# Optimization experiments

Hardware: AMD Instinct MI355X
Metric: run time of the kernel (lower is better)

## Reference

```python
import jax, jax.numpy as jnp
import numpy as np

N_GRAPHS, NODES_PER, DEG, D = 128, 1024, 32, 256
N = N_GRAPHS * NODES_PER          # 131072 nodes
E = N * DEG                       # 4194304 edges
RATIO = 0.8
K = int(np.ceil(RATIO * NODES_PER))  # 820 nodes kept per graph


def setup_inputs() -> dict:
    key = jax.random.key(0)
    k1, k2, k3, k4 = jax.random.split(key, 4)
    x = jax.random.normal(k1, (N, D), dtype=jnp.float32)
    # intra-graph random edges: endpoints within [0, NODES_PER) + graph offset
    src = jax.random.randint(k2, (E,), 0, NODES_PER)
    dst = jax.random.randint(k3, (E,), 0, NODES_PER)
    goff = (jnp.arange(E) // (NODES_PER * DEG)) * NODES_PER
    edge_index = jnp.stack([src + goff, dst + goff]).astype(jnp.int32)
    batch = jnp.repeat(jnp.arange(N_GRAPHS, dtype=jnp.int32), NODES_PER)
    W = jax.random.normal(k4, (D, 1), dtype=jnp.float32) / np.sqrt(D)
    b = jnp.zeros((1,), dtype=jnp.float32)
    return {"x": x, "edge_index": edge_index, "batch": batch, "W": W, "b": b}


def _gcn_score(x, edge_index, W, b):
    # GCNConv(in_channels, 1) with added self-loops and symmetric normalization
    n = x.shape[0]
    row, col = edge_index[0], edge_index[1]  # source, target
    # degree at target, init 1.0 accounts for self-loop
    deg = jnp.ones((n,), x.dtype).at[col].add(jnp.ones_like(col, dtype=x.dtype))
    dinv = jax.lax.rsqrt(deg)
    h = x @ W                                 # [n, 1]
    norm = dinv[row] * dinv[col]              # [E]
    agg = jnp.zeros_like(h).at[col].add(norm[:, None] * h[row])
    agg = agg + (dinv * dinv)[:, None] * h    # self-loop contribution deg^-1 * h_i
    return (agg + b).squeeze(-1)              # [n]


def reference(x, edge_index, batch, W, b):
    score = _gcn_score(x, edge_index, W, b)                     # [N]
    # per-graph top-k (graphs are contiguous, equal size)
    score_g = score.reshape(N_GRAPHS, NODES_PER)
    _, idx = jax.lax.top_k(score_g, K)                          # [G, K]
    perm = (idx + jnp.arange(N_GRAPHS)[:, None] * NODES_PER).reshape(-1)  # [G*K]
    x_new = x[perm] * jnp.tanh(score[perm])[:, None]            # [G*K, D]
    batch_new = batch[perm]
    # filter_adj: remap kept nodes to new ids, mask edges with dropped endpoints
    new_id = jnp.full((x.shape[0],), -1, dtype=perm.dtype).at[perm].set(
        jnp.arange(perm.shape[0], dtype=perm.dtype))
    r2 = new_id[edge_index[0]]
    c2 = new_id[edge_index[1]]
    edge_mask = (r2 >= 0) & (c2 >= 0)                           # [E] valid edges
    edge_index_new = jnp.where(edge_mask, jnp.stack([r2, c2]), -1)  # [2, E], -1 = dropped
    return x_new, edge_index_new, edge_mask, batch_new, perm
```

## Files before the change

kernel.cpp:

```cpp
#include <hip/hip_runtime.h>
#include <math.h>

constexpr int NG    = 128;
constexpr int NP    = 1024;
constexpr int D     = 256;
constexpr int NTOT  = NG * NP;
constexpr int EPG   = NP * 32;
constexpr int ET    = NTOT * 32;
constexpr int KK    = 820;
constexpr int NKEEP = NG * KK;
constexpr int BPG   = 4;
constexpr int EPB   = EPG / BPG;
constexpr int NBE   = NG * BPG;

constexpr int K1_BLOCKS = 2048;
constexpr int K3_BLOCKS = 2048;

typedef float v4f __attribute__((ext_vector_type(4)));

constexpr long long OUT_X     = 0;
constexpr long long OUT_EI0   = (long long)NKEEP * D;
constexpr long long OUT_EI1   = OUT_EI0 + ET;
constexpr long long OUT_MASK  = OUT_EI0 + 2LL * ET;
constexpr long long OUT_BATCH = OUT_MASK + ET;
constexpr long long OUT_PERM  = OUT_BATCH + NKEEP;

__global__ __launch_bounds__(256) void k1_h(const float* __restrict__ x,
                                            const float* __restrict__ W,
                                            float* __restrict__ h,
                                            int* __restrict__ new_id) {
    const int t    = threadIdx.x;
    const int w    = t >> 6;
    const int lane = t & 63;
    const int gw   = blockIdx.x * 4 + w;

    float4 w4 = ((const float4*)W)[lane];
    const float4* xp = (const float4*)(x + (size_t)gw * 16 * D);

#pragma unroll
    for (int c = 0; c < 4; ++c) {
        float4 a0 = xp[(c * 4 + 0) * 64 + lane];
        float4 a1 = xp[(c * 4 + 1) * 64 + lane];
        float4 a2 = xp[(c * 4 + 2) * 64 + lane];
        float4 a3 = xp[(c * 4 + 3) * 64 + lane];
        float s0 = a0.x * w4.x + a0.y * w4.y + a0.z * w4.z + a0.w * w4.w;
        float s1 = a1.x * w4.x + a1.y * w4.y + a1.z * w4.z + a1.w * w4.w;
        float s2 = a2.x * w4.x + a2.y * w4.y + a2.z * w4.z + a2.w * w4.w;
        float s3 = a3.x * w4.x + a3.y * w4.y + a3.z * w4.z + a3.w * w4.w;
#pragma unroll
        for (int off = 32; off > 0; off >>= 1) {
            s0 += __shfl_down(s0, off, 64);
            s1 += __shfl_down(s1, off, 64);
            s2 += __shfl_down(s2, off, 64);
            s3 += __shfl_down(s3, off, 64);
        }
        if (lane == 0) {
            const int r = gw * 16 + c * 4;
            h[r] = s0; h[r + 1] = s1; h[r + 2] = s2; h[r + 3] = s3;
            new_id[r]     = -1; new_id[r + 1] = -1;
            new_id[r + 2] = -1; new_id[r + 3] = -1;
        }
    }
}

__global__ __launch_bounds__(1024) void k2_graph(
        const float* __restrict__ h,  const float* __restrict__ bptr,
        const int* __restrict__ rows, const int* __restrict__ cols,
        int* __restrict__ perm_i,     int* __restrict__ new_id,
        float* __restrict__ factor,
        float* __restrict__ out_perm, float* __restrict__ out_batch) {
    __shared__ unsigned long long sk[NP];
    __shared__ float acc[NP];
    __shared__ float scl[NP];
    int*   cnt = (int*)sk;
    float* ul  = (float*)sk + NP;

    const int g = blockIdx.x;
    const int t = threadIdx.x;

    const float hv = h[g * NP + t];
    cnt[t] = 0;
    __syncthreads();

    const int4* c4 = (const int4*)(cols + (size_t)g * EPG);
    const int4* r4 = (const int4*)(rows + (size_t)g * EPG);

#pragma unroll
    for (int i = t; i < EPG / 4; i += 1024) {
        int4 c = c4[i];
        atomicAdd(&cnt[c.x & (NP - 1)], 1);
        atomicAdd(&cnt[c.y & (NP - 1)], 1);
        atomicAdd(&cnt[c.z & (NP - 1)], 1);
        atomicAdd(&cnt[c.w & (NP - 1)], 1);
    }
    __syncthreads();

    const float di = rsqrtf((float)(1 + cnt[t]));
    ul[t]  = di * hv;
    acc[t] = 0.0f;
    __syncthreads();

#pragma unroll
    for (int i = t; i < EPG / 4; i += 1024) {
        int4 c = c4[i];
        int4 r = r4[i];
        atomicAdd(&acc[c.x & (NP - 1)], ul[r.x & (NP - 1)]);
        atomicAdd(&acc[c.y & (NP - 1)], ul[r.y & (NP - 1)]);
        atomicAdd(&acc[c.z & (NP - 1)], ul[r.z & (NP - 1)]);
        atomicAdd(&acc[c.w & (NP - 1)], ul[r.w & (NP - 1)]);
    }
    __syncthreads();

    const float score = di * acc[t] + di * di * hv + bptr[0];
    scl[t] = score;

    unsigned int fu = __float_as_uint(score);
    unsigned int s  = (fu & 0x80000000u) ? ~fu : (fu | 0x80000000u);
    unsigned long long key = ((unsigned long long)(~s) << 32) | (unsigned int)t;

    for (int k = 2; k <= NP; k <<= 1) {
        for (int j = k >> 1; j > 0; j >>= 1) {
            unsigned long long other;
            if (j < 64) {
                other = __shfl_xor(key, j, 64);
            } else {
                sk[t] = key;
                __syncthreads();
                other = sk[t ^ j];
                __syncthreads();
            }
            bool take_min = (((t & k) == 0) == ((t & j) == 0));
            bool omin = other < key;
            key = (take_min == omin) ? other : key;
        }
    }

    if (t < KK) {
        int idx  = (int)(key & 0xFFFFFFFFull);
        int node = g * NP + idx;
        int j    = g * KK + t;
        perm_i[j]    = node;
        new_id[node] = j;
        out_perm[j]  = (float)node;
        out_batch[j] = (float)g;
        factor[j]    = tanhf(scl[idx]);
    }
}

__global__ __launch_bounds__(256) void k3_gather_edge(
        const float* __restrict__ x,
        const int* __restrict__ rows, const int* __restrict__ cols,
        const int* __restrict__ new_id,
        const int* __restrict__ perm_i, const float* __restrict__ factor,
        float* __restrict__ out) {
    __shared__ int nid[NP];
    const int b    = blockIdx.x;
    const int t    = threadIdx.x;
    const int w    = t >> 6;
    const int lane = t & 63;

    if (b < NBE) {
        const int g = b >> 2;
        for (int i = t; i < NP; i += 256) nid[i] = new_id[g * NP + i];
        __syncthreads();
        size_t eoff = (size_t)g * EPG + (size_t)(b & 3) * EPB;
        const int4* r4 = (const int4*)(rows + eoff);
        const int4* c4 = (const int4*)(cols + eoff);
        v4f* orr = (v4f*)(out + OUT_EI0  + eoff);
        v4f* occ = (v4f*)(out + OUT_EI1  + eoff);
        v4f* omm = (v4f*)(out + OUT_MASK + eoff);
#pragma unroll
        for (int i = t; i < EPB / 4; i += 256) {
            int4 r = r4[i];
            int4 c = c4[i];
            v4f fr, fc, fm;
            {
                int nr = nid[r.x & (NP - 1)], nc = nid[c.x & (NP - 1)];
                bool m = (nr >= 0) && (nc >= 0);
                fr.x = m ? (float)nr : -1.0f; fc.x = m ? (float)nc : -1.0f; fm.x = m ? 1.0f : 0.0f;
            }
            {
                int nr = nid[r.y & (NP - 1)], nc = nid[c.y & (NP - 1)];
                bool m = (nr >= 0) && (nc >= 0);
                fr.y = m ? (float)nr : -1.0f; fc.y = m ? (float)nc : -1.0f; fm.y = m ? 1.0f : 0.0f;
            }
            {
                int nr = nid[r.z & (NP - 1)], nc = nid[c.z & (NP - 1)];
                bool m = (nr >= 0) && (nc >= 0);
                fr.z = m ? (float)nr : -1.0f; fc.z = m ? (float)nc : -1.0f; fm.z = m ? 1.0f : 0.0f;
            }
            {
                int nr = nid[r.w & (NP - 1)], nc = nid[c.w & (NP - 1)];
                bool m = (nr >= 0) && (nc >= 0);
                fr.w = m ? (float)nr : -1.0f; fc.w = m ? (float)nc : -1.0f; fm.w = m ? 1.0f : 0.0f;
            }
            __builtin_nontemporal_store(fr, &orr[i]);
            __builtin_nontemporal_store(fc, &occ[i]);
            __builtin_nontemporal_store(fm, &omm[i]);
        }
    } else {
        const int gw = (b - NBE) * 4 + w;
        for (int j = gw; j < NKEEP; j += (K3_BLOCKS - NBE) * 4) {
            const int node = perm_i[j];
            const float f  = factor[j];
            float4 v = ((const float4*)(x + (size_t)node * D))[lane];
            v4f o;
            o.x = v.x * f; o.y = v.y * f; o.z = v.z * f; o.w = v.w * f;
            __builtin_nontemporal_store(o, &((v4f*)(out + OUT_X + (size_t)j * D))[lane]);
        }
    }
}

extern "C" void kernel_launch(void* const* d_in, const int* in_sizes, int n_in,
                              void* d_out, int out_size, void* d_ws, size_t ws_size,
                              hipStream_t stream) {
    (void)in_sizes; (void)n_in; (void)out_size; (void)ws_size;

    const float* x  = (const float*)d_in[0];
    const int*   ei = (const int*)d_in[1];
    const float* W  = (const float*)d_in[3];
    const float* b  = (const float*)d_in[4];
    float* out = (float*)d_out;

    float* wsf      = (float*)d_ws;
    float* h        = wsf;
    int*   new_id   = (int*)(wsf + NTOT);
    int*   perm_i   = (int*)(wsf + 2 * NTOT);
    float* factor   = wsf + 2 * NTOT + NKEEP;

    const int* rows = ei;
    const int* cols = ei + ET;

    hipLaunchKernelGGL(k1_h, dim3(K1_BLOCKS), dim3(256), 0, stream,
                       x, W, h, new_id);
    hipLaunchKernelGGL(k2_graph, dim3(NG), dim3(1024), 0, stream,
                       h, b, rows, cols, perm_i, new_id, factor,
                       out + OUT_PERM, out + OUT_BATCH);
    hipLaunchKernelGGL(k3_gather_edge, dim3(K3_BLOCKS), dim3(256), 0, stream,
                       x, rows, cols, new_id, perm_i, factor, out);
}
```

Measured before the change: 350.5 us.

## Fuse score, top-k, gather and edge filter into one per-graph kernel

```diff
diff --git a/kernel.cpp b/kernel.cpp
--- a/kernel.cpp
+++ b/kernel.cpp
@@ -8,13 +8,9 @@
 constexpr int EPG   = NP * 32;
 constexpr int ET    = NTOT * 32;
 constexpr int KK    = 820;
+constexpr int KH    = KK / 2;
 constexpr int NKEEP = NG * KK;
-constexpr int BPG   = 4;
-constexpr int EPB   = EPG / BPG;
-constexpr int NBE   = NG * BPG;
-
-constexpr int K1_BLOCKS = 2048;
-constexpr int K3_BLOCKS = 2048;
+constexpr int EHALF = EPG / 2;
 
 typedef float v4f __attribute__((ext_vector_type(4)));
 
@@ -25,69 +21,66 @@
 constexpr long long OUT_BATCH = OUT_MASK + ET;
 constexpr long long OUT_PERM  = OUT_BATCH + NKEEP;
 
-__global__ __launch_bounds__(256) void k1_h(const float* __restrict__ x,
-                                            const float* __restrict__ W,
-                                            float* __restrict__ h,
-                                            int* __restrict__ new_id) {
+__global__ __launch_bounds__(1024) void sagpool_fused(
+        const float* __restrict__ x,   const float* __restrict__ W,
+        const float* __restrict__ bptr,
+        const int* __restrict__ rows,  const int* __restrict__ cols,
+        float* __restrict__ out) {
+    __shared__ float h_lds[NP];
+    __shared__ unsigned long long sk[NP];
+    __shared__ float acc[NP];
+    __shared__ float scl[NP];
+    __shared__ int   nid[NP];
+    int*   cnt  = (int*)sk;
+    float* ul   = (float*)sk + NP;
+    int*   kidx = (int*)h_lds;
+    float* kfac = acc;
+
+    const int blk  = blockIdx.x;
     const int t    = threadIdx.x;
     const int w    = t >> 6;
     const int lane = t & 63;
-    const int gw   = blockIdx.x * 4 + w;
-
-    float4 w4 = ((const float4*)W)[lane];
-    const float4* xp = (const float4*)(x + (size_t)gw * 16 * D);
-
-#pragma unroll
-    for (int c = 0; c < 4; ++c) {
-        float4 a0 = xp[(c * 4 + 0) * 64 + lane];
-        float4 a1 = xp[(c * 4 + 1) * 64 + lane];
-        float4 a2 = xp[(c * 4 + 2) * 64 + lane];
-        float4 a3 = xp[(c * 4 + 3) * 64 + lane];
-        float s0 = a0.x * w4.x + a0.y * w4.y + a0.z * w4.z + a0.w * w4.w;
-        float s1 = a1.x * w4.x + a1.y * w4.y + a1.z * w4.z + a1.w * w4.w;
-        float s2 = a2.x * w4.x + a2.y * w4.y + a2.z * w4.z + a2.w * w4.w;
-        float s3 = a3.x * w4.x + a3.y * w4.y + a3.z * w4.z + a3.w * w4.w;
-#pragma unroll
-        for (int off = 32; off > 0; off >>= 1) {
-            s0 += __shfl_down(s0, off, 64);
-            s1 += __shfl_down(s1, off, 64);
-            s2 += __shfl_down(s2, off, 64);
-            s3 += __shfl_down(s3, off, 64);
-        }
-        if (lane == 0) {
-            const int r = gw * 16 + c * 4;
-            h[r] = s0; h[r + 1] = s1; h[r + 2] = s2; h[r + 3] = s3;
-            new_id[r]     = -1; new_id[r + 1] = -1;
-            new_id[r + 2] = -1; new_id[r + 3] = -1;
-        }
-    }
-}
-
-__global__ __launch_bounds__(1024) void k2_graph(
-        const float* __restrict__ h,  const float* __restrict__ bptr,
-        const int* __restrict__ rows, const int* __restrict__ cols,
-        int* __restrict__ perm_i,     int* __restrict__ new_id,
-        float* __restrict__ factor,
-        float* __restrict__ out_perm, float* __restrict__ out_batch) {
-    __shared__ unsigned long long sk[NP];
-    __shared__ float acc[NP];
-    __shared__ float scl[NP];
-    int*   cnt = (int*)sk;
-    float* ul  = (float*)sk + NP;
-
-    const int g = blockIdx.x;
-    const int t = threadIdx.x;
-
-    const float hv = h[g * NP + t];
+    const int g    = blk >> 1;
+    const int half = blk & 1;
+
     cnt[t] = 0;
-    __syncthreads();
-
-    const int4* c4 = (const int4*)(cols + (size_t)g * EPG);
-    const int4* r4 = (const int4*)(rows + (size_t)g * EPG);
+    nid[t] = -1;
+
+    {
+        float4 w4 = ((const float4*)W)[lane];
+        const float4* xp = (const float4*)(x + (size_t)g * NP * D);
+#pragma unroll
+        for (int c = 0; c < 16; ++c) {
+            const int r0 = w * 64 + c * 4;
+            float4 a0 = xp[(r0 + 0) * 64 + lane];
+            float4 a1 = xp[(r0 + 1) * 64 + lane];
+            float4 a2 = xp[(r0 + 2) * 64 + lane];
+            float4 a3 = xp[(r0 + 3) * 64 + lane];
+            float s0 = a0.x * w4.x + a0.y * w4.y + a0.z * w4.z + a0.w * w4.w;
+            float s1 = a1.x * w4.x + a1.y * w4.y + a1.z * w4.z + a1.w * w4.w;
+            float s2 = a2.x * w4.x + a2.y * w4.y + a2.z * w4.z + a2.w * w4.w;
+            float s3 = a3.x * w4.x + a3.y * w4.y + a3.z * w4.z + a3.w * w4.w;
+#pragma unroll
+            for (int off = 32; off > 0; off >>= 1) {
+                s0 += __shfl_down(s0, off, 64);
+                s1 += __shfl_down(s1, off, 64);
+                s2 += __shfl_down(s2, off, 64);
+                s3 += __shfl_down(s3, off, 64);
+            }
+            if (lane == 0) {
+                h_lds[r0]     = s0; h_lds[r0 + 1] = s1;
+                h_lds[r0 + 2] = s2; h_lds[r0 + 3] = s3;
+            }
+        }
+    }
+    __syncthreads();
+
+    const int4* c4p = (const int4*)(cols + (size_t)g * EPG);
+    const int4* r4p = (const int4*)(rows + (size_t)g * EPG);
 
 #pragma unroll
     for (int i = t; i < EPG / 4; i += 1024) {
-        int4 c = c4[i];
+        int4 c = c4p[i];
         atomicAdd(&cnt[c.x & (NP - 1)], 1);
         atomicAdd(&cnt[c.y & (NP - 1)], 1);
         atomicAdd(&cnt[c.z & (NP - 1)], 1);
@@ -95,6 +88,7 @@
     }
     __syncthreads();
 
+    const float hv = h_lds[t];
     const float di = rsqrtf((float)(1 + cnt[t]));
     ul[t]  = di * hv;
     acc[t] = 0.0f;
@@ -102,8 +96,8 @@
 
 #pragma unroll
     for (int i = t; i < EPG / 4; i += 1024) {
-        int4 c = c4[i];
-        int4 r = r4[i];
+        int4 c = c4p[i];
+        int4 r = r4p[i];
         atomicAdd(&acc[c.x & (NP - 1)], ul[r.x & (NP - 1)]);
         atomicAdd(&acc[c.y & (NP - 1)], ul[r.y & (NP - 1)]);
         atomicAdd(&acc[c.z & (NP - 1)], ul[r.z & (NP - 1)]);
@@ -137,40 +131,37 @@
 
     if (t < KK) {
         int idx  = (int)(key & 0xFFFFFFFFull);
-        int node = g * NP + idx;
-        int j    = g * KK + t;
-        perm_i[j]    = node;
-        new_id[node] = j;
-        out_perm[j]  = (float)node;
-        out_batch[j] = (float)g;
-        factor[j]    = tanhf(scl[idx]);
-    }
-}
-
-__global__ __launch_bounds__(256) void k3_gather_edge(
-        const float* __restrict__ x,
-        const int* __restrict__ rows, const int* __restrict__ cols,
-        const int* __restrict__ new_id,
-        const int* __restrict__ perm_i, const float* __restrict__ factor,
-        float* __restrict__ out) {
-    __shared__ int nid[NP];
-    const int b    = blockIdx.x;
-    const int t    = threadIdx.x;
-    const int w    = t >> 6;
-    const int lane = t & 63;
-
-    if (b < NBE) {
-        const int g = b >> 2;
-        for (int i = t; i < NP; i += 256) nid[i] = new_id[g * NP + i];
-        __syncthreads();
-        size_t eoff = (size_t)g * EPG + (size_t)(b & 3) * EPB;
+        nid[idx] = g * KK + t;
+        if (t >= half * KH && t < half * KH + KH) {
+            const int l = t - half * KH;
+            kidx[l] = idx;
+            kfac[l] = tanhf(scl[idx]);
+            const int jj = g * KK + t;
+            out[OUT_PERM + jj]  = (float)(g * NP + idx);
+            out[OUT_BATCH + jj] = (float)g;
+        }
+    }
+    __syncthreads();
+
+    for (int l = w; l < KH; l += 16) {
+        const int   ni = kidx[l];
+        const float f  = kfac[l];
+        float4 v = ((const float4*)(x + ((size_t)(g * NP + ni)) * D))[lane];
+        v4f o;
+        o.x = v.x * f; o.y = v.y * f; o.z = v.z * f; o.w = v.w * f;
+        const size_t j = (size_t)g * KK + half * KH + l;
+        __builtin_nontemporal_store(o, &((v4f*)(out + OUT_X + j * D))[lane]);
+    }
+
+    {
+        const size_t eoff = (size_t)g * EPG + (size_t)half * EHALF;
         const int4* r4 = (const int4*)(rows + eoff);
         const int4* c4 = (const int4*)(cols + eoff);
         v4f* orr = (v4f*)(out + OUT_EI0  + eoff);
         v4f* occ = (v4f*)(out + OUT_EI1  + eoff);
         v4f* omm = (v4f*)(out + OUT_MASK + eoff);
 #pragma unroll
-        for (int i = t; i < EPB / 4; i += 256) {
+        for (int i = t; i < EHALF / 4; i += 1024) {
             int4 r = r4[i];
             int4 c = c4[i];
             v4f fr, fc, fm;
@@ -198,23 +189,13 @@
             __builtin_nontemporal_store(fc, &occ[i]);
             __builtin_nontemporal_store(fm, &omm[i]);
         }
-    } else {
-        const int gw = (b - NBE) * 4 + w;
-        for (int j = gw; j < NKEEP; j += (K3_BLOCKS - NBE) * 4) {
-            const int node = perm_i[j];
-            const float f  = factor[j];
-            float4 v = ((const float4*)(x + (size_t)node * D))[lane];
-            v4f o;
-            o.x = v.x * f; o.y = v.y * f; o.z = v.z * f; o.w = v.w * f;
-            __builtin_nontemporal_store(o, &((v4f*)(out + OUT_X + (size_t)j * D))[lane]);
-        }
     }
 }
 
 extern "C" void kernel_launch(void* const* d_in, const int* in_sizes, int n_in,
                               void* d_out, int out_size, void* d_ws, size_t ws_size,
                               hipStream_t stream) {
-    (void)in_sizes; (void)n_in; (void)out_size; (void)ws_size;
+    (void)in_sizes; (void)n_in; (void)out_size; (void)d_ws; (void)ws_size;
 
     const float* x  = (const float*)d_in[0];
     const int*   ei = (const int*)d_in[1];
@@ -222,20 +203,9 @@
     const float* b  = (const float*)d_in[4];
     float* out = (float*)d_out;
 
-    float* wsf      = (float*)d_ws;
-    float* h        = wsf;
-    int*   new_id   = (int*)(wsf + NTOT);
-    int*   perm_i   = (int*)(wsf + 2 * NTOT);
-    float* factor   = wsf + 2 * NTOT + NKEEP;
-
     const int* rows = ei;
     const int* cols = ei + ET;
 
-    hipLaunchKernelGGL(k1_h, dim3(K1_BLOCKS), dim3(256), 0, stream,
-                       x, W, h, new_id);
-    hipLaunchKernelGGL(k2_graph, dim3(NG), dim3(1024), 0, stream,
-                       h, b, rows, cols, perm_i, new_id, factor,
-                       out + OUT_PERM, out + OUT_BATCH);
-    hipLaunchKernelGGL(k3_gather_edge, dim3(K3_BLOCKS), dim3(256), 0, stream,
-                       x, rows, cols, new_id, perm_i, factor, out);
+    hipLaunchKernelGGL(sagpool_fused, dim3(2 * NG), dim3(1024), 0, stream,
+                       x, W, b, rows, cols, out);
 }
```

After: 348.5 us. About the same (-0.6%).

## Move degree counting into the first kernel alongside the x@W projection

Applied to the files above, without the earlier changes.

```diff
diff --git a/kernel.cpp b/kernel.cpp
--- a/kernel.cpp
+++ b/kernel.cpp
@@ -13,7 +13,9 @@
 constexpr int EPB   = EPG / BPG;
 constexpr int NBE   = NG * BPG;
 
-constexpr int K1_BLOCKS = 2048;
+constexpr int K1_DEG    = NG;
+constexpr int K1_HBLK   = 2048;
+constexpr int K1_BLOCKS = K1_DEG + K1_HBLK;
 constexpr int K3_BLOCKS = 2048;
 
 typedef float v4f __attribute__((ext_vector_type(4)));
@@ -25,18 +27,40 @@
 constexpr long long OUT_BATCH = OUT_MASK + ET;
 constexpr long long OUT_PERM  = OUT_BATCH + NKEEP;
 
-__global__ __launch_bounds__(256) void k1_h(const float* __restrict__ x,
-                                            const float* __restrict__ W,
-                                            float* __restrict__ h,
-                                            int* __restrict__ new_id) {
-    const int t    = threadIdx.x;
+__global__ __launch_bounds__(256) void k1_h_deg(const float* __restrict__ x,
+                                                const float* __restrict__ W,
+                                                const int* __restrict__ cols,
+                                                float* __restrict__ h,
+                                                float* __restrict__ dinv) {
+    __shared__ int cnt[NP];
+    const int b = blockIdx.x;
+    const int t = threadIdx.x;
+
+    if (b < K1_DEG) {
+        const int g = b;
+        for (int i = t; i < NP; i += 256) cnt[i] = 0;
+        __syncthreads();
+        const int4* c4 = (const int4*)(cols + (size_t)g * EPG);
+#pragma unroll
+        for (int i = t; i < EPG / 4; i += 256) {
+            int4 c = c4[i];
+            atomicAdd(&cnt[c.x & (NP - 1)], 1);
+            atomicAdd(&cnt[c.y & (NP - 1)], 1);
+            atomicAdd(&cnt[c.z & (NP - 1)], 1);
+            atomicAdd(&cnt[c.w & (NP - 1)], 1);
+        }
+        __syncthreads();
+        for (int i = t; i < NP; i += 256)
+            dinv[g * NP + i] = rsqrtf((float)(1 + cnt[i]));
+        return;
+    }
+
+    const int bb   = b - K1_DEG;
     const int w    = t >> 6;
     const int lane = t & 63;
-    const int gw   = blockIdx.x * 4 + w;
-
+    const int gw   = bb * 4 + w;
     float4 w4 = ((const float4*)W)[lane];
     const float4* xp = (const float4*)(x + (size_t)gw * 16 * D);
-
 #pragma unroll
     for (int c = 0; c < 4; ++c) {
         float4 a0 = xp[(c * 4 + 0) * 64 + lane];
@@ -57,49 +81,33 @@
         if (lane == 0) {
             const int r = gw * 16 + c * 4;
             h[r] = s0; h[r + 1] = s1; h[r + 2] = s2; h[r + 3] = s3;
-            new_id[r]     = -1; new_id[r + 1] = -1;
-            new_id[r + 2] = -1; new_id[r + 3] = -1;
         }
     }
 }
 
 __global__ __launch_bounds__(1024) void k2_graph(
-        const float* __restrict__ h,  const float* __restrict__ bptr,
-        const int* __restrict__ rows, const int* __restrict__ cols,
-        int* __restrict__ perm_i,     int* __restrict__ new_id,
-        float* __restrict__ factor,
-        float* __restrict__ out_perm, float* __restrict__ out_batch) {
+        const float* __restrict__ h,    const float* __restrict__ dinv,
+        const float* __restrict__ bptr,
+        const int* __restrict__ rows,   const int* __restrict__ cols,
+        int* __restrict__ perm_i,       float* __restrict__ factor,
+        int* __restrict__ new_id,
+        float* __restrict__ out_perm,   float* __restrict__ out_batch) {
     __shared__ unsigned long long sk[NP];
     __shared__ float acc[NP];
     __shared__ float scl[NP];
-    int*   cnt = (int*)sk;
-    float* ul  = (float*)sk + NP;
+    float* ul = (float*)sk;
 
     const int g = blockIdx.x;
     const int t = threadIdx.x;
 
     const float hv = h[g * NP + t];
-    cnt[t] = 0;
+    const float dv = dinv[g * NP + t];
+    ul[t]  = dv * hv;
+    acc[t] = 0.0f;
     __syncthreads();
 
     const int4* c4 = (const int4*)(cols + (size_t)g * EPG);
     const int4* r4 = (const int4*)(rows + (size_t)g * EPG);
-
-#pragma unroll
-    for (int i = t; i < EPG / 4; i += 1024) {
-        int4 c = c4[i];
-        atomicAdd(&cnt[c.x & (NP - 1)], 1);
-        atomicAdd(&cnt[c.y & (NP - 1)], 1);
-        atomicAdd(&cnt[c.z & (NP - 1)], 1);
-        atomicAdd(&cnt[c.w & (NP - 1)], 1);
-    }
-    __syncthreads();
-
-    const float di = rsqrtf((float)(1 + cnt[t]));
-    ul[t]  = di * hv;
-    acc[t] = 0.0f;
-    __syncthreads();
-
 #pragma unroll
     for (int i = t; i < EPG / 4; i += 1024) {
         int4 c = c4[i];
@@ -111,7 +119,7 @@
     }
     __syncthreads();
 
-    const float score = di * acc[t] + di * di * hv + bptr[0];
+    const float score = dv * acc[t] + dv * dv * hv + bptr[0];
     scl[t] = score;
 
     unsigned int fu = __float_as_uint(score);
@@ -135,15 +143,16 @@
         }
     }
 
+    const int idx = (int)(key & 0xFFFFFFFFull);
     if (t < KK) {
-        int idx  = (int)(key & 0xFFFFFFFFull);
-        int node = g * NP + idx;
-        int j    = g * KK + t;
-        perm_i[j]    = node;
-        new_id[node] = j;
-        out_perm[j]  = (float)node;
-        out_batch[j] = (float)g;
-        factor[j]    = tanhf(scl[idx]);
+        const int jj = g * KK + t;
+        new_id[g * NP + idx] = jj;
+        perm_i[jj]   = g * NP + idx;
+        factor[jj]   = tanhf(scl[idx]);
+        out_perm[jj]  = (float)(g * NP + idx);
+        out_batch[jj] = (float)g;
+    } else {
+        new_id[g * NP + idx] = -1;
     }
 }
 
@@ -224,17 +233,18 @@
 
     float* wsf      = (float*)d_ws;
     float* h        = wsf;
-    int*   new_id   = (int*)(wsf + NTOT);
-    int*   perm_i   = (int*)(wsf + 2 * NTOT);
-    float* factor   = wsf + 2 * NTOT + NKEEP;
+    float* dinv     = wsf + NTOT;
+    int*   new_id   = (int*)(wsf + 2 * NTOT);
+    int*   perm_i   = (int*)(wsf + 3 * NTOT);
+    float* factor   = wsf + 3 * NTOT + NKEEP;
 
     const int* rows = ei;
     const int* cols = ei + ET;
 
-    hipLaunchKernelGGL(k1_h, dim3(K1_BLOCKS), dim3(256), 0, stream,
-                       x, W, h, new_id);
+    hipLaunchKernelGGL(k1_h_deg, dim3(K1_BLOCKS), dim3(256), 0, stream,
+                       x, W, cols, h, dinv);
     hipLaunchKernelGGL(k2_graph, dim3(NG), dim3(1024), 0, stream,
-                       h, b, rows, cols, perm_i, new_id, factor,
+                       h, dinv, b, rows, cols, perm_i, factor, new_id,
                        out + OUT_PERM, out + OUT_BATCH);
     hipLaunchKernelGGL(k3_gather_edge, dim3(K3_BLOCKS), dim3(256), 0, stream,
                        x, rows, cols, new_id, perm_i, factor, out);
```

Result: no change. 354.0 us (+1.0%).
